# Performance work log

Hardware: AMD Instinct MI355X
Metric: run time of the kernel (lower is better)

## Reference

```python
import jax, jax.numpy as jnp
import numpy as np

D_MODEL = 1024
PATCH = 16
HID = 256
VOCAB = 256

def setup_inputs() -> dict:
    key = jax.random.key(0)
    ks = jax.random.split(key, 12)
    B, N = 16, 512
    s = lambda *sh: 1.0 / np.sqrt(sh[-1])
    inp = {
        'latents': jax.random.normal(ks[0], (B, N, D_MODEL), dtype=jnp.float32),
        'target_bytes': jax.random.randint(ks[1], (B, N * PATCH), 0, VOCAB, dtype=jnp.int64),
        'W_proj': jax.random.normal(ks[2], (HID, D_MODEL), dtype=jnp.float32) * s(HID, D_MODEL),
        'b_proj': jnp.zeros((HID,), dtype=jnp.float32),
        'emb_table': jax.random.normal(ks[3], (VOCAB, HID), dtype=jnp.float32),
        'W_ih': jax.random.normal(ks[4], (3 * HID, 2 * HID), dtype=jnp.float32) * s(1, 2 * HID),
        'W_hh': jax.random.normal(ks[5], (3 * HID, HID), dtype=jnp.float32) * s(1, HID),
        'b_ih': jnp.zeros((3 * HID,), dtype=jnp.float32),
        'b_hh': jnp.zeros((3 * HID,), dtype=jnp.float32),
        'W_head': jax.random.normal(ks[6], (VOCAB, HID), dtype=jnp.float32) * s(VOCAB, HID),
        'b_head': jnp.zeros((VOCAB,), dtype=jnp.float32),
    }
    return inp

def _gru_scan(x_proj, W_hh, b_hh, h0):
    # x_proj: [T, BN, 3H] precomputed input projections (incl. b_ih)
    def step(h, xg):
        hg = h @ W_hh.T + b_hh                      # [BN, 3H]
        xr, xz, xn = jnp.split(xg, 3, axis=-1)
        hr, hz, hn = jnp.split(hg, 3, axis=-1)
        r = jax.nn.sigmoid(xr + hr)
        z = jax.nn.sigmoid(xz + hz)
        n = jnp.tanh(xn + r * hn)
        h_new = (1.0 - z) * n + z * h
        return h_new, h_new
    _, outs = jax.lax.scan(step, h0, x_proj)
    return outs                                      # [T, BN, H]

def reference(latents, target_bytes, W_proj, b_proj, emb_table, W_ih, W_hh, b_ih, b_hh, W_head, b_head):
    B, N, D = latents.shape
    BN = B * N
    latent_ctx = (latents.reshape(BN, D) @ W_proj.T + b_proj)        # [BN, H]
    targets = target_bytes.reshape(BN, PATCH)
    sos = jnp.zeros((BN, 1), dtype=targets.dtype)
    rnn_in_bytes = jnp.concatenate([sos, targets[:, :-1]], axis=1)   # [BN, P]
    emb = emb_table[rnn_in_bytes]                                    # [BN, P, H]
    lat_exp = jnp.broadcast_to(latent_ctx[:, None, :], (BN, PATCH, HID))
    rnn_input = jnp.concatenate([emb, lat_exp], axis=-1)             # [BN, P, 2H]
    x_proj = jnp.einsum('bpi,gi->bpg', rnn_input, W_ih) + b_ih       # [BN, P, 3H]
    h0 = jnp.zeros((BN, HID), dtype=latents.dtype)
    outs = _gru_scan(jnp.swapaxes(x_proj, 0, 1), W_hh, b_hh, h0)     # [P, BN, H]
    outs = jnp.swapaxes(outs, 0, 1)                                  # [BN, P, H]
    logits = jnp.einsum('bph,vh->bpv', outs, W_head) + b_head        # [BN, P, 256]
    return logits.reshape(B, N, PATCH, VOCAB)
```

## Files before the change

### kernel.cpp

```cpp
#include <hip/hip_runtime.h>
#include <math.h>

#define NSEQ 8192
#define PATCHL 16
#define HIDN 256
#define VOCABN 256

typedef __attribute__((ext_vector_type(4))) float f32x4;
typedef __attribute__((ext_vector_type(8))) short bf16x8;

__device__ __forceinline__ unsigned short f2bf(float f) {
    unsigned int x = __float_as_uint(f);
    unsigned int r = (x + 0x7fffu + ((x >> 16) & 1u)) >> 16;
    return (unsigned short)r;
}
__device__ __forceinline__ float bf2f(unsigned short b) {
    return __uint_as_float(((unsigned int)b) << 16);
}
__device__ __forceinline__ float sigf(float x)   { return 1.f / (1.f + __expf(-x)); }
__device__ __forceinline__ float tanhf_(float x) { return 2.f / (1.f + __expf(-2.f * x)) - 1.f; }

__global__ __launch_bounds__(256)
void pack_frag(const float* __restrict__ src, int ld, int col0, int nks,
               unsigned short* __restrict__ dst)
{
    const int g = blockIdx.x * 256 + threadIdx.x;
    const int lane = g & 63;
    const int ks = (g / 64) % nks;
    const int T  = g / (64 * nks);
    const float* s = src + (size_t)(T * 16 + (lane & 15)) * ld + col0 + ks * 32 + ((lane >> 4) & 3) * 8;
    unsigned int q[4];
#pragma unroll
    for (int j = 0; j < 4; j++) {
        unsigned int lo = f2bf(s[2 * j]);
        unsigned int hi = f2bf(s[2 * j + 1]);
        q[j] = lo | (hi << 16);
    }
    uint4 v; v.x = q[0]; v.y = q[1]; v.z = q[2]; v.w = q[3];
    *(uint4*)(dst + (size_t)g * 8) = v;
}

template<bool ASRC_BF16, int OUT_MODE>
__global__ __launch_bounds__(512)
void gemm_mfma(const void* __restrict__ Asrc, int lda,
               const unsigned short* __restrict__ bpack, int nks_total,
               const float* __restrict__ bias, void* __restrict__ Cdst, int ldc,
               int K)
{
    const int tid = threadIdx.x;
    const int w = tid >> 6, lane = tid & 63;
    const int l15 = lane & 15, kg = (lane >> 4) & 3;
    const int bm = blockIdx.x * 128, bn = blockIdx.y * 64;

    __shared__ unsigned short As[2][128 * 64];

    const int srow = tid >> 2;
    const int scol = (tid & 3) * 16;
    const int nkt = K / 64;

    f32x4 acc[4];
#pragma unroll
    for (int nt = 0; nt < 4; nt++) acc[nt] = 0.f;

    const int wb0 = srow * 128 + ((scol * 2) ^ ((srow & 7) << 4));
    const int wb1 = srow * 128 + ((scol * 2 + 16) ^ ((srow & 7) << 4));

#define STAGE(kt, buf) do {                                                         \
        const int gk = (kt) * 64 + scol;                                            \
        unsigned short tmp[16];                                                     \
        if (ASRC_BF16) {                                                            \
            const unsigned short* A = (const unsigned short*)Asrc;                  \
            *(uint4*)(tmp)     = *(const uint4*)(A + (size_t)(bm + srow) * lda + gk);      \
            *(uint4*)(tmp + 8) = *(const uint4*)(A + (size_t)(bm + srow) * lda + gk + 8);  \
        } else {                                                                    \
            const float* A = (const float*)Asrc;                                    \
            const float4 a0 = *(const float4*)(A + (size_t)(bm + srow) * lda + gk);       \
            const float4 a1 = *(const float4*)(A + (size_t)(bm + srow) * lda + gk + 4);   \
            const float4 a2 = *(const float4*)(A + (size_t)(bm + srow) * lda + gk + 8);   \
            const float4 a3 = *(const float4*)(A + (size_t)(bm + srow) * lda + gk + 12);  \
            tmp[0] = f2bf(a0.x);  tmp[1] = f2bf(a0.y);  tmp[2] = f2bf(a0.z);  tmp[3] = f2bf(a0.w);   \
            tmp[4] = f2bf(a1.x);  tmp[5] = f2bf(a1.y);  tmp[6] = f2bf(a1.z);  tmp[7] = f2bf(a1.w);   \
            tmp[8] = f2bf(a2.x);  tmp[9] = f2bf(a2.y);  tmp[10] = f2bf(a2.z); tmp[11] = f2bf(a2.w);  \
            tmp[12] = f2bf(a3.x); tmp[13] = f2bf(a3.y); tmp[14] = f2bf(a3.z); tmp[15] = f2bf(a3.w);  \
        }                                                                           \
        *(uint4*)((char*)As[buf] + wb0) = *(uint4*)tmp;                             \
        *(uint4*)((char*)As[buf] + wb1) = *(uint4*)(tmp + 8);                       \
    } while (0)

    STAGE(0, 0);
    __syncthreads();

    for (int kt = 0; kt < nkt; ++kt) {
        if (kt + 1 < nkt) STAGE(kt + 1, (kt + 1) & 1);
        const unsigned short* buf = As[kt & 1];
        const int row = w * 16 + l15;
#pragma unroll
        for (int ks = 0; ks < 2; ++ks) {
            const int bo = row * 128 + (((ks * 64) + kg * 16) ^ ((row & 7) << 4));
            const bf16x8 a = *(const bf16x8*)((const char*)buf + bo);
#pragma unroll
            for (int nt = 0; nt < 4; ++nt) {
                const int T = blockIdx.y * 4 + nt;
                const bf16x8 b = *(const bf16x8*)(bpack + (((size_t)T * nks_total + (kt * 2 + ks)) * 64 + lane) * 8);
                acc[nt] = __builtin_amdgcn_mfma_f32_16x16x32_bf16(a, b, acc[nt], 0, 0, 0);
            }
        }
        __syncthreads();
    }
#undef STAGE

#pragma unroll
    for (int nt = 0; nt < 4; ++nt) {
        const int n = bn + nt * 16 + l15;
        const float bv = bias ? bias[n] : 0.f;
#pragma unroll
        for (int rr = 0; rr < 4; ++rr) {
            const int m = bm + w * 16 + kg * 4 + rr;
            const float v = acc[nt][rr] + bv;
            if (OUT_MODE == 0)      ((float*)Cdst)[(size_t)m * ldc + n] = v;
            else if (OUT_MODE == 1) ((unsigned short*)Cdst)[(size_t)m * ldc + n] = f2bf(v);
            else                    ((unsigned short*)Cdst)[(size_t)m * 1024 + (n & 255) * 4 + (n >> 8)] = f2bf(v);
        }
    }
}

#define G4S 1032
__global__ __launch_bounds__(512)
void gru_scan_fused(const int* __restrict__ bytes,
                    const unsigned short* __restrict__ latg4,
                    const unsigned short* __restrict__ pmx4,
                    const unsigned short* __restrict__ wpack,
                    const float* __restrict__ b_hh,
                    unsigned short* __restrict__ hh,
                    int seq0)
{
    const int tid  = threadIdx.x;
    const int w    = tid >> 6;
    const int lane = tid & 63;
    const int l15  = lane & 15;
    const int kg   = (lane >> 4) & 3;
    const int s0l  = blockIdx.x * 32;
    const int s0g  = seq0 + s0l;

    __shared__ unsigned short LG[32 * G4S];
    __shared__ unsigned short H[32 * 256];
    __shared__ int BYs[512];

    BYs[tid] = bytes[(size_t)s0g * PATCHL + tid];

#pragma unroll
    for (int j = 0; j < 8; ++j) {
        const int idx = j * 512 + tid;
        const int row = idx >> 7, col = idx & 127;
        *(uint4*)(LG + row * G4S + col * 8) =
            *(const uint4*)(latg4 + (size_t)(s0g + row) * 1024 + col * 8);
    }

    float bhr[2], bhz[2], bhn[2];
#pragma unroll
    for (int nt = 0; nt < 2; nt++) {
        const int u = w * 32 + nt * 16 + l15;
        bhr[nt] = b_hh[u]; bhz[nt] = b_hh[256 + u]; bhn[nt] = b_hh[512 + u];
    }

    float hreg[2][2][4];
#pragma unroll
    for (int mt = 0; mt < 2; mt++)
#pragma unroll
        for (int nt = 0; nt < 2; nt++)
#pragma unroll
            for (int rr = 0; rr < 4; rr++) hreg[mt][nt][rr] = 0.f;

    __syncthreads();

#define MFMA_GATE(gg, acc) do {                                                     \
        _Pragma("unroll")                                                           \
        for (int ks = 0; ks < 8; ks += 2) {                                         \
            bf16x8 B[2][2];                                                         \
            _Pragma("unroll")                                                       \
            for (int dk = 0; dk < 2; ++dk)                                          \
                _Pragma("unroll")                                                   \
                for (int nt = 0; nt < 2; ++nt) {                                    \
                    const int T = (gg) * 16 + w * 2 + nt;                           \
                    B[dk][nt] = *(const bf16x8*)(wpack + (((size_t)T * 8 + ks + dk) * 64 + lane) * 8); \
                }                                                                   \
            _Pragma("unroll")                                                       \
            for (int dk = 0; dk < 2; ++dk)                                          \
                _Pragma("unroll")                                                   \
                for (int mt = 0; mt < 2; ++mt) {                                    \
                    const int s = mt * 16 + l15;                                    \
                    const int off = ((ks + dk) * 64 + kg * 16) ^ ((l15 & 7) << 4);  \
                    const bf16x8 a = *(const bf16x8*)(H + s * 256 + (off >> 1));    \
                    _Pragma("unroll")                                               \
                    for (int nt = 0; nt < 2; ++nt)                                  \
                        acc[mt][nt] = __builtin_amdgcn_mfma_f32_16x16x32_bf16(a, B[dk][nt], acc[mt][nt], 0, 0, 0); \
                }                                                                   \
        }                                                                           \
    } while (0)

    for (int p = 0; p < PATCHL; ++p) {
        ushort4 pmreg[2][2][4];
#pragma unroll
        for (int mt = 0; mt < 2; mt++)
#pragma unroll
            for (int nt = 0; nt < 2; nt++) {
                const int u = w * 32 + nt * 16 + l15;
#pragma unroll
                for (int rr = 0; rr < 4; rr++) {
                    const int sl = mt * 16 + kg * 4 + rr;
                    const int bv = p ? BYs[sl * PATCHL + p - 1] : 0;
                    pmreg[mt][nt][rr] = *(const ushort4*)(pmx4 + (size_t)bv * 1024 + u * 4);
                }
            }

        if (p) {
#pragma unroll
            for (int rj = 0; rj < 4; ++rj) {
                const int row = w * 4 + rj;
                const int boff = (lane * 8) ^ ((row & 7) << 4);
                const ushort4 v = *(const ushort4*)((const char*)(H + row * 256) + boff);
                *(ushort4*)(hh + ((size_t)(s0l + row) * PATCHL + (p - 1)) * 256 + lane * 4) = v;
            }
        }

        f32x4 acc[2][2];
#pragma unroll
        for (int mt = 0; mt < 2; mt++)
#pragma unroll
            for (int nt = 0; nt < 2; nt++) acc[mt][nt] = 0.f;
        if (p) MFMA_GATE(0, acc);

        float rv[2][2][4], xz[2][2][4], xn[2][2][4];
#pragma unroll
        for (int mt = 0; mt < 2; mt++)
#pragma unroll
            for (int nt = 0; nt < 2; nt++) {
                const int u = w * 32 + nt * 16 + l15;
#pragma unroll
                for (int rr = 0; rr < 4; rr++) {
                    const int sl = mt * 16 + kg * 4 + rr;
                    const ushort4 lg4 = *(const ushort4*)(LG + sl * G4S + u * 4);
                    const ushort4 pm4 = pmreg[mt][nt][rr];
                    const float xr = bf2f(lg4.x) + bf2f(pm4.x) + bhr[nt];
                    rv[mt][nt][rr] = sigf(xr + acc[mt][nt][rr]);
                    xz[mt][nt][rr] = bf2f(lg4.y) + bf2f(pm4.y) + bhz[nt];
                    xn[mt][nt][rr] = bf2f(lg4.z) + bf2f(pm4.z);
                }
            }

#pragma unroll
        for (int mt = 0; mt < 2; mt++)
#pragma unroll
            for (int nt = 0; nt < 2; nt++) acc[mt][nt] = 0.f;
        if (p) MFMA_GATE(1, acc);

        float zv[2][2][4];
#pragma unroll
        for (int mt = 0; mt < 2; mt++)
#pragma unroll
            for (int nt = 0; nt < 2; nt++)
#pragma unroll
                for (int rr = 0; rr < 4; rr++)
                    zv[mt][nt][rr] = sigf(xz[mt][nt][rr] + acc[mt][nt][rr]);

#pragma unroll
        for (int mt = 0; mt < 2; mt++)
#pragma unroll
            for (int nt = 0; nt < 2; nt++) acc[mt][nt] = 0.f;
        if (p) MFMA_GATE(2, acc);

        __syncthreads();

#pragma unroll
        for (int mt = 0; mt < 2; mt++)
#pragma unroll
            for (int nt = 0; nt < 2; nt++) {
                const int u = w * 32 + nt * 16 + l15;
#pragma unroll
                for (int rr = 0; rr < 4; rr++) {
                    const int sl = mt * 16 + kg * 4 + rr;
                    const float n = tanhf_(xn[mt][nt][rr] + rv[mt][nt][rr] * (acc[mt][nt][rr] + bhn[nt]));
                    const float hn_ = (1.f - zv[mt][nt][rr]) * n + zv[mt][nt][rr] * hreg[mt][nt][rr];
                    hreg[mt][nt][rr] = hn_;
                    const int bo = (2 * u) ^ ((sl & 7) << 4);
                    H[sl * 256 + (bo >> 1)] = f2bf(hn_);
                }
            }
        __syncthreads();
    }
#undef MFMA_GATE

#pragma unroll
    for (int rj = 0; rj < 4; ++rj) {
        const int row = w * 4 + rj;
        const int boff = (lane * 8) ^ ((row & 7) << 4);
        const ushort4 v = *(const ushort4*)((const char*)(H + row * 256) + boff);
        *(ushort4*)(hh + ((size_t)(s0l + row) * PATCHL + (PATCHL - 1)) * 256 + lane * 4) = v;
    }
}

extern "C" void kernel_launch(void* const* d_in, const int* in_sizes, int n_in,
                              void* d_out, int out_size, void* d_ws, size_t ws_size,
                              hipStream_t stream)
{
    const float* latents = (const float*)d_in[0];
    const int*   tb      = (const int*)d_in[1];
    const float* W_proj  = (const float*)d_in[2];
    const float* b_proj  = (const float*)d_in[3];
    const float* emb     = (const float*)d_in[4];
    const float* W_ih    = (const float*)d_in[5];
    const float* W_hh    = (const float*)d_in[6];
    const float* b_ih    = (const float*)d_in[7];
    const float* b_hh    = (const float*)d_in[8];
    const float* W_head  = (const float*)d_in[9];
    const float* b_head  = (const float*)d_in[10];
    float* out = (float*)d_out;

    char* w = (char*)d_ws;
    unsigned short* latg4   = (unsigned short*)w;          w += (size_t)NSEQ * 1024 * 2;
    unsigned short* ctxb    = (unsigned short*)w;          w += (size_t)NSEQ * HIDN * 2;
    unsigned short* pmx4    = (unsigned short*)w;          w += 256 * 1024 * 2;
    unsigned short* bpack1  = (unsigned short*)w;          w += 16 * 32 * 64 * 8 * 2;
    unsigned short* bpack2  = (unsigned short*)w;          w += 48 * 8 * 64 * 8 * 2;
    unsigned short* bpack3  = (unsigned short*)w;          w += 48 * 8 * 64 * 8 * 2;
    unsigned short* wpackG  = (unsigned short*)w;          w += 48 * 8 * 64 * 8 * 2;
    unsigned short* bpackH  = (unsigned short*)w;          w += 16 * 8 * 64 * 8 * 2;
    unsigned short* hh_c    = (unsigned short*)w;
    const size_t fixed_bytes = (size_t)(w - (char*)d_ws);
    const size_t chunk_full  = (size_t)NSEQ * PATCHL * 256 * 2;

    int nch = 1;
    while (nch < 16 && fixed_bytes + chunk_full / nch > ws_size) nch <<= 1;
    const int SPC = NSEQ / nch;

    hipLaunchKernelGGL(pack_frag, dim3(128), dim3(256), 0, stream, W_proj, 1024, 0, 32, bpack1);
    hipLaunchKernelGGL(pack_frag, dim3(96),  dim3(256), 0, stream, W_ih,   512, 256, 8, bpack2);
    hipLaunchKernelGGL(pack_frag, dim3(96),  dim3(256), 0, stream, W_ih,   512, 0,   8, bpack3);
    hipLaunchKernelGGL(pack_frag, dim3(96),  dim3(256), 0, stream, W_hh,   256, 0,   8, wpackG);
    hipLaunchKernelGGL(pack_frag, dim3(32),  dim3(256), 0, stream, W_head, 256, 0,   8, bpackH);

    hipLaunchKernelGGL((gemm_mfma<false, 2>), dim3(2, 12), dim3(512), 0, stream,
                       emb, 256, bpack3, 8, nullptr, pmx4, 1024, 256);
    hipLaunchKernelGGL((gemm_mfma<false, 1>), dim3(NSEQ / 128, 4), dim3(512), 0, stream,
                       latents, 1024, bpack1, 32, b_proj, ctxb, 256, 1024);
    hipLaunchKernelGGL((gemm_mfma<true, 2>), dim3(NSEQ / 128, 12), dim3(512), 0, stream,
                       ctxb, 256, bpack2, 8, b_ih, latg4, 1024, 256);

    for (int c = 0; c < nch; ++c) {
        const int seq0 = c * SPC;
        hipLaunchKernelGGL(gru_scan_fused, dim3(SPC / 32), dim3(512), 0, stream,
                           tb, latg4, pmx4, wpackG, b_hh, hh_c, seq0);
        hipLaunchKernelGGL((gemm_mfma<true, 0>), dim3(SPC * PATCHL / 128, 4), dim3(512), 0, stream,
                           hh_c, 256, bpackH, 8, b_head,
                           out + (size_t)seq0 * PATCHL * VOCABN, 256, 256);
    }
}
```

Measured before the change: 349.6 us.

## Fuse output head GEMM into GRU scan with double-buffered hidden state

Runs the vocabulary head projection inside the GRU scan kernel: each step's hidden state in shared memory is multiplied by the packed W_head fragments and the fp32 logits go straight to the output. This drops the bf16 hidden-state write and read through global memory, along with the separate head GEMM launch and the chunking loop. The hidden state is double-buffered in LDS so one barrier per step is removed. In exchange the scan kernel does more MFMA work per step and uses more LDS, which can lower occupancy, and its output stores are strided fp32 writes from fragment layout.

```diff
diff --git a/kernel.cpp b/kernel.cpp
--- a/kernel.cpp
+++ b/kernel.cpp
@@ -130,37 +130,39 @@
                     const unsigned short* __restrict__ latg4,
                     const unsigned short* __restrict__ pmx4,
                     const unsigned short* __restrict__ wpack,
+                    const unsigned short* __restrict__ hpack,
                     const float* __restrict__ b_hh,
-                    unsigned short* __restrict__ hh,
-                    int seq0)
+                    const float* __restrict__ b_head,
+                    float* __restrict__ out)
 {
     const int tid  = threadIdx.x;
     const int w    = tid >> 6;
     const int lane = tid & 63;
     const int l15  = lane & 15;
     const int kg   = (lane >> 4) & 3;
-    const int s0l  = blockIdx.x * 32;
-    const int s0g  = seq0 + s0l;
-
+    const int s0   = blockIdx.x * 32;
+
+    __shared__ unsigned short H0[32 * 256];
+    __shared__ unsigned short H1[32 * 256];
     __shared__ unsigned short LG[32 * G4S];
-    __shared__ unsigned short H[32 * 256];
     __shared__ int BYs[512];
 
-    BYs[tid] = bytes[(size_t)s0g * PATCHL + tid];
+    BYs[tid] = bytes[(size_t)s0 * PATCHL + tid];
 
 #pragma unroll
     for (int j = 0; j < 8; ++j) {
         const int idx = j * 512 + tid;
         const int row = idx >> 7, col = idx & 127;
         *(uint4*)(LG + row * G4S + col * 8) =
-            *(const uint4*)(latg4 + (size_t)(s0g + row) * 1024 + col * 8);
-    }
-
-    float bhr[2], bhz[2], bhn[2];
+            *(const uint4*)(latg4 + (size_t)(s0 + row) * 1024 + col * 8);
+    }
+
+    float bhr[2], bhz[2], bhn[2], bhd[2];
 #pragma unroll
     for (int nt = 0; nt < 2; nt++) {
         const int u = w * 32 + nt * 16 + l15;
         bhr[nt] = b_hh[u]; bhz[nt] = b_hh[256 + u]; bhn[nt] = b_hh[512 + u];
+        bhd[nt] = b_head[u];
     }
 
     float hreg[2][2][4];
@@ -171,9 +173,12 @@
 #pragma unroll
             for (int rr = 0; rr < 4; rr++) hreg[mt][nt][rr] = 0.f;
 
+    unsigned short* Hcur = H0;
+    unsigned short* Hnxt = H1;
+
     __syncthreads();
 
-#define MFMA_GATE(gg, acc) do {                                                     \
+#define MFMA_TILES(pk, tbase, Hb, acc) do {                                         \
         _Pragma("unroll")                                                           \
         for (int ks = 0; ks < 8; ks += 2) {                                         \
             bf16x8 B[2][2];                                                         \
@@ -181,8 +186,8 @@
             for (int dk = 0; dk < 2; ++dk)                                          \
                 _Pragma("unroll")                                                   \
                 for (int nt = 0; nt < 2; ++nt) {                                    \
-                    const int T = (gg) * 16 + w * 2 + nt;                           \
-                    B[dk][nt] = *(const bf16x8*)(wpack + (((size_t)T * 8 + ks + dk) * 64 + lane) * 8); \
+                    const int T = (tbase) + w * 2 + nt;                             \
+                    B[dk][nt] = *(const bf16x8*)((pk) + (((size_t)T * 8 + ks + dk) * 64 + lane) * 8); \
                 }                                                                   \
             _Pragma("unroll")                                                       \
             for (int dk = 0; dk < 2; ++dk)                                          \
@@ -190,7 +195,7 @@
                 for (int mt = 0; mt < 2; ++mt) {                                    \
                     const int s = mt * 16 + l15;                                    \
                     const int off = ((ks + dk) * 64 + kg * 16) ^ ((l15 & 7) << 4);  \
-                    const bf16x8 a = *(const bf16x8*)(H + s * 256 + (off >> 1));    \
+                    const bf16x8 a = *(const bf16x8*)((Hb) + s * 256 + (off >> 1)); \
                     _Pragma("unroll")                                               \
                     for (int nt = 0; nt < 2; ++nt)                                  \
                         acc[mt][nt] = __builtin_amdgcn_mfma_f32_16x16x32_bf16(a, B[dk][nt], acc[mt][nt], 0, 0, 0); \
@@ -198,6 +203,27 @@
         }                                                                           \
     } while (0)
 
+#define HEAD_STORE(pp, Hb) do {                                                     \
+        f32x4 acch[2][2];                                                           \
+        _Pragma("unroll")                                                           \
+        for (int mt = 0; mt < 2; mt++)                                              \
+            _Pragma("unroll")                                                       \
+            for (int nt = 0; nt < 2; nt++) acch[mt][nt] = 0.f;                      \
+        MFMA_TILES(hpack, 0, Hb, acch);                                             \
+        _Pragma("unroll")                                                           \
+        for (int mt = 0; mt < 2; mt++)                                              \
+            _Pragma("unroll")                                                       \
+            for (int nt = 0; nt < 2; nt++) {                                        \
+                const int u = w * 32 + nt * 16 + l15;                               \
+                _Pragma("unroll")                                                   \
+                for (int rr = 0; rr < 4; rr++) {                                    \
+                    const int sl = mt * 16 + kg * 4 + rr;                           \
+                    out[((size_t)(s0 + sl) * PATCHL + (pp)) * VOCABN + u] =         \
+                        acch[mt][nt][rr] + bhd[nt];                                 \
+                }                                                                   \
+            }                                                                       \
+    } while (0)
+
     for (int p = 0; p < PATCHL; ++p) {
         ushort4 pmreg[2][2][4];
 #pragma unroll
@@ -213,22 +239,14 @@
                 }
             }
 
-        if (p) {
-#pragma unroll
-            for (int rj = 0; rj < 4; ++rj) {
-                const int row = w * 4 + rj;
-                const int boff = (lane * 8) ^ ((row & 7) << 4);
-                const ushort4 v = *(const ushort4*)((const char*)(H + row * 256) + boff);
-                *(ushort4*)(hh + ((size_t)(s0l + row) * PATCHL + (p - 1)) * 256 + lane * 4) = v;
-            }
-        }
+        if (p) HEAD_STORE(p - 1, Hcur);
 
         f32x4 acc[2][2];
 #pragma unroll
         for (int mt = 0; mt < 2; mt++)
 #pragma unroll
             for (int nt = 0; nt < 2; nt++) acc[mt][nt] = 0.f;
-        if (p) MFMA_GATE(0, acc);
+        if (p) MFMA_TILES(wpack, 0, Hcur, acc);
 
         float rv[2][2][4], xz[2][2][4], xn[2][2][4];
 #pragma unroll
@@ -252,7 +270,7 @@
         for (int mt = 0; mt < 2; mt++)
 #pragma unroll
             for (int nt = 0; nt < 2; nt++) acc[mt][nt] = 0.f;
-        if (p) MFMA_GATE(1, acc);
+        if (p) MFMA_TILES(wpack, 16, Hcur, acc);
 
         float zv[2][2][4];
 #pragma unroll
@@ -267,9 +285,7 @@
         for (int mt = 0; mt < 2; mt++)
 #pragma unroll
             for (int nt = 0; nt < 2; nt++) acc[mt][nt] = 0.f;
-        if (p) MFMA_GATE(2, acc);
-
-        __syncthreads();
+        if (p) MFMA_TILES(wpack, 32, Hcur, acc);
 
 #pragma unroll
         for (int mt = 0; mt < 2; mt++)
@@ -283,20 +299,16 @@
                     const float hn_ = (1.f - zv[mt][nt][rr]) * n + zv[mt][nt][rr] * hreg[mt][nt][rr];
                     hreg[mt][nt][rr] = hn_;
                     const int bo = (2 * u) ^ ((sl & 7) << 4);
-                    H[sl * 256 + (bo >> 1)] = f2bf(hn_);
+                    Hnxt[sl * 256 + (bo >> 1)] = f2bf(hn_);
                 }
             }
         __syncthreads();
-    }
-#undef MFMA_GATE
-
-#pragma unroll
-    for (int rj = 0; rj < 4; ++rj) {
-        const int row = w * 4 + rj;
-        const int boff = (lane * 8) ^ ((row & 7) << 4);
-        const ushort4 v = *(const ushort4*)((const char*)(H + row * 256) + boff);
-        *(ushort4*)(hh + ((size_t)(s0l + row) * PATCHL + (PATCHL - 1)) * 256 + lane * 4) = v;
-    }
+        unsigned short* t_ = Hcur; Hcur = Hnxt; Hnxt = t_;
+    }
+
+    HEAD_STORE(PATCHL - 1, Hcur);
+#undef HEAD_STORE
+#undef MFMA_TILES
 }
 
 extern "C" void kernel_launch(void* const* d_in, const int* in_sizes, int n_in,
@@ -325,13 +337,6 @@
     unsigned short* bpack3  = (unsigned short*)w;          w += 48 * 8 * 64 * 8 * 2;
     unsigned short* wpackG  = (unsigned short*)w;          w += 48 * 8 * 64 * 8 * 2;
     unsigned short* bpackH  = (unsigned short*)w;          w += 16 * 8 * 64 * 8 * 2;
-    unsigned short* hh_c    = (unsigned short*)w;
-    const size_t fixed_bytes = (size_t)(w - (char*)d_ws);
-    const size_t chunk_full  = (size_t)NSEQ * PATCHL * 256 * 2;
-
-    int nch = 1;
-    while (nch < 16 && fixed_bytes + chunk_full / nch > ws_size) nch <<= 1;
-    const int SPC = NSEQ / nch;
 
     hipLaunchKernelGGL(pack_frag, dim3(128), dim3(256), 0, stream, W_proj, 1024, 0, 32, bpack1);
     hipLaunchKernelGGL(pack_frag, dim3(96),  dim3(256), 0, stream, W_ih,   512, 256, 8, bpack2);
@@ -346,12 +351,6 @@
     hipLaunchKernelGGL((gemm_mfma<true, 2>), dim3(NSEQ / 128, 12), dim3(512), 0, stream,
                        ctxb, 256, bpack2, 8, b_ih, latg4, 1024, 256);
 
-    for (int c = 0; c < nch; ++c) {
-        const int seq0 = c * SPC;
-        hipLaunchKernelGGL(gru_scan_fused, dim3(SPC / 32), dim3(512), 0, stream,
-                           tb, latg4, pmx4, wpackG, b_hh, hh_c, seq0);
-        hipLaunchKernelGGL((gemm_mfma<true, 0>), dim3(SPC * PATCHL / 128, 4), dim3(512), 0, stream,
-                           hh_c, 256, bpackH, 8, b_head,
-                           out + (size_t)seq0 * PATCHL * VOCABN, 256, 256);
-    }
-}
+    hipLaunchKernelGGL(gru_scan_fused, dim3(NSEQ / 32), dim3(512), 0, stream,
+                       tb, latg4, pmx4, wpackG, bpackH, b_hh, b_head, out);
+}
```

Result: slower. 375.3 us (+7.3%).
